# Optimization experiments

Measured on AMD Instinct MI355X. Metric: run time of the kernel, lower is better.

The kernel has to match this reference:

```python
import jax, jax.numpy as jnp
import numpy as np

N = 50000          # nodes
E_RAND = 590000    # random edges (+ N self-loops -> E = 640000)
IN_F = 128
OUT_F = 128
H, D = 8, 16       # num_heads, head_dim (H*D == OUT_F)
HOP = 5
ALPHA = 0.1
SLOPE = 0.2
EPS = 1e-5


def _layer_norm(x, g, b):
    mu = jnp.mean(x, axis=-1, keepdims=True)
    var = jnp.mean((x - mu) ** 2, axis=-1, keepdims=True)
    return (x - mu) * jax.lax.rsqrt(var + EPS) * g + b


def setup_inputs() -> dict:
    key = jax.random.key(0)
    ks = jax.random.split(key, 10)
    loops = jnp.arange(N, dtype=jnp.int32)  # self-loops -> no 0-in-degree nodes
    src = jnp.concatenate([loops, jax.random.randint(ks[0], (E_RAND,), 0, N, dtype=jnp.int32)])
    dst = jnp.concatenate([loops, jax.random.randint(ks[1], (E_RAND,), 0, N, dtype=jnp.int32)])
    s = 0.05  # xavier-like small init gain
    return {
        "feat": jax.random.normal(ks[2], (N, IN_F), jnp.float32),
        "src": src,
        "dst": dst,
        "w_head": jax.random.normal(ks[3], (OUT_F, IN_F), jnp.float32) * s,
        "w_tail": jax.random.normal(ks[4], (OUT_F, IN_F), jnp.float32) * s,
        "w_ent": jax.random.normal(ks[5], (OUT_F, IN_F), jnp.float32) * s,
        "attn": jax.random.normal(ks[6], (1, H, D), jnp.float32) * s,
        "ln1_g": jnp.ones((IN_F,), jnp.float32),
        "ln1_b": jnp.zeros((IN_F,), jnp.float32),
        "ln2_g": jnp.ones((OUT_F,), jnp.float32),
        "ln2_b": jnp.zeros((OUT_F,), jnp.float32),
        "ff_w1": jax.random.normal(ks[7], (4 * OUT_F, OUT_F), jnp.float32) * s,
        "ff_b1": jnp.zeros((4 * OUT_F,), jnp.float32),
        "ff_w2": jax.random.normal(ks[8], (OUT_F, 4 * OUT_F), jnp.float32) * s,
        "ff_b2": jnp.zeros((OUT_F,), jnp.float32),
    }


def _forward(src, dst, feat, w_head, w_tail, w_ent, attn,
             ln1_g, ln1_b, ln2_g, ln2_b, ff_w1, ff_b1, ff_w2, ff_b2):
    ones = jnp.ones(src.shape[0], jnp.float32)
    out_deg = jnp.clip(jax.ops.segment_sum(ones, src, num_segments=N), 1.0)  # [N]
    in_deg = jnp.clip(jax.ops.segment_sum(ones, dst, num_segments=N), 1.0)
    head_norm = out_deg ** -0.5
    tail_norm = in_deg ** 0.5
    log_in = jnp.log1p(in_deg)  # graph.dstdata['log_in'] (log of in-degree, set at graph build time)

    x = _layer_norm(feat, ln1_g, ln1_b)  # graph_layer_norm (feat_drop=0 in eval)
    fh = (x @ w_head.T).reshape(N, H, D) * head_norm[:, None, None]
    ft = (x @ w_tail.T).reshape(N, H, D) * head_norm[:, None, None]
    fe = (x @ w_ent.T).reshape(N, H, D) * head_norm[:, None, None]

    # edge attention logits: u_mul_v -> leaky_relu -> dot with attn vector
    lr = jax.nn.leaky_relu(fh[src] * ft[dst], SLOPE)  # [E,H,D]
    e = jnp.einsum('ehd,xhd->eh', lr, attn)           # [E,H]
    e = e * log_in[dst][:, None] / D                  # e_mul_v with log_in, / head_dim

    # edge softmax grouped by destination node, per head
    seg_max = jax.ops.segment_max(e, dst, num_segments=N)
    e_exp = jnp.exp(e - seg_max[dst])
    denom = jax.ops.segment_sum(e_exp, dst, num_segments=N)
    a = e_exp / denom[dst]                            # [E,H]

    # PPR diffusion (ppr_estimation), attn_drop=0 in eval
    feat0 = fe
    h = feat0
    for hop in range(HOP):
        if hop > 0:
            h = h * head_norm[:, None, None]
        m = h[src] * a[:, :, None]                    # [E,H,D] u_mul_e
        h = jax.ops.segment_sum(m, dst, num_segments=N)  # fn.sum
        h = h * tail_norm[:, None, None]
        h = (1.0 - ALPHA) * h + ALPHA * feat0

    rst = h + feat.reshape(N, H, D)  # res_fc is Identity since in_feats == out_feats
    rst = rst.reshape(N, OUT_F)
    ff = _layer_norm(rst, ln2_g, ln2_b)
    ff = jax.nn.relu(ff @ ff_w1.T + ff_b1) @ ff_w2.T + ff_b2  # PositionWiseFeedForward
    return ff + rst


def reference(feat, src, dst, w_head, w_tail, w_ent, attn, ln1_g, ln1_b,
              ln2_g, ln2_b, ff_w1, ff_b1, ff_w2, ff_b2):
    return _forward(src, dst, feat, w_head, w_tail, w_ent, attn,
                    ln1_g, ln1_b, ln2_g, ln2_b, ff_w1, ff_b1, ff_w2, ff_b2)
```

## Files before the change

### kernel.cpp

```cpp
#include <hip/hip_runtime.h>
#include <hip/hip_bf16.h>

typedef __attribute__((ext_vector_type(8))) short bf16x8;
typedef __attribute__((ext_vector_type(4))) float f32x4;
typedef unsigned int uint32;

#define F 128
#define HOPS 5
#define LDS_STRIDE 68
#define W1_STRIDE 136
#define W2_STRIDE 72
#define TB_STRIDE 72

__device__ __forceinline__ float b2f(__hip_bfloat16 h) { return __bfloat162float(h); }
__device__ __forceinline__ __hip_bfloat16 f2b(float f) { return __float2bfloat16(f); }

__device__ __forceinline__ float load_in(const void* p, size_t i, int isbf) {
    return isbf ? __bfloat162float(((const __hip_bfloat16*)p)[i]) : ((const float*)p)[i];
}

__device__ __forceinline__ float bflo(uint32 u) { union { uint32 i; float f; } v; v.i = u << 16; return v.f; }
__device__ __forceinline__ float bfhi(uint32 u) { union { uint32 i; float f; } v; v.i = u & 0xffff0000u; return v.f; }
__device__ __forceinline__ uint32 packbf2(float a, float b) {
    __hip_bfloat16 ha = f2b(a), hb = f2b(b);
    unsigned short ua = *(unsigned short*)&ha, ub = *(unsigned short*)&hb;
    return ((uint32)ub << 16) | ua;
}

__device__ __forceinline__ float edge_dot(uint4 gv, const float* ftf, const float* at) {
    float acc = 0.f;
    uint32 us[4] = {gv.x, gv.y, gv.z, gv.w};
    #pragma unroll
    for (int k = 0; k < 4; ++k) {
        float f0 = bflo(us[k]) * ftf[2 * k];
        float f1 = bfhi(us[k]) * ftf[2 * k + 1];
        f0 = fmaxf(f0, 0.2f * f0);
        f1 = fmaxf(f1, 0.2f * f1);
        acc = fmaf(f0, at[2 * k], acc);
        acc = fmaf(f1, at[2 * k + 1], acc);
    }
    return acc;
}

__global__ void detect_k(const uint32* __restrict__ w, int* flag) {
    __shared__ int cnt[256];
    int t = threadIdx.x;
    uint32 x = w[t * 97];
    int e_low = (x >> 7) & 0xFF;
    cnt[t] = (e_low >= 110 && e_low <= 135) ? 1 : 0;
    __syncthreads();
    for (int s = 128; s > 0; s >>= 1) {
        if (t < s) cnt[t] += cnt[t + s];
        __syncthreads();
    }
    if (t == 0) flag[0] = (cnt[0] >= 160) ? 1 : 0;
}

__global__ void cvt_all_k(const void* __restrict__ w_head, const void* __restrict__ w_tail,
                          const void* __restrict__ w_ent, const void* __restrict__ ff_w1,
                          const void* __restrict__ ff_w2, const void* __restrict__ attn,
                          const void* __restrict__ ff_b1, const void* __restrict__ ff_b2,
                          const int* __restrict__ flag,
                          __hip_bfloat16* __restrict__ wblob, float* __restrict__ fblob) {
    int i = blockIdx.x * blockDim.x + threadIdx.x;
    int isbf = flag[0];
    if (i < 180224) {
        const void* srcp; int j;
        if (i < 16384)       { srcp = w_head; j = i; }
        else if (i < 32768)  { srcp = w_tail; j = i - 16384; }
        else if (i < 49152)  { srcp = w_ent;  j = i - 32768; }
        else if (i < 114688) { srcp = ff_w1;  j = i - 49152; }
        else                 { srcp = ff_w2;  j = i - 114688; }
        wblob[i] = f2b(load_in(srcp, j, isbf));
    } else if (i < 180992) {
        int k = i - 180224;
        const void* srcp; int j;
        if (k < 128)      { srcp = attn;  j = k; }
        else if (k < 640) { srcp = ff_b1; j = k - 128; }
        else              { srcp = ff_b2; j = k - 640; }
        fblob[k] = load_in(srcp, j, isbf);
    }
}

__global__ void degree_k(const int* __restrict__ src, const int* __restrict__ dst,
                         int* in_cnt, int* out_cnt, int E) {
    int i = blockIdx.x * blockDim.x + threadIdx.x;
    if (i < E) {
        atomicAdd(&in_cnt[dst[i]], 1);
        atomicAdd(&out_cnt[src[i]], 1);
    }
}

__global__ void scan1_k(const int* __restrict__ cnt, int* partial, int* blk_sum, int N) {
    __shared__ int sh[256];
    int t = threadIdx.x;
    int i = blockIdx.x * 256 + t;
    int c = (i < N) ? cnt[i] : 0;
    sh[t] = c;
    __syncthreads();
    for (int o = 1; o < 256; o <<= 1) {
        int v = (t >= o) ? sh[t - o] : 0;
        __syncthreads();
        sh[t] += v;
        __syncthreads();
    }
    if (i < N) partial[i] = sh[t] - c;
    if (t == 255) blk_sum[blockIdx.x] = sh[255];
}

__global__ void scan2_k(const int* __restrict__ blk_sum, int* blk_off, int nb,
                        int* row_ptr, int N) {
    __shared__ int sh[256];
    int t = threadIdx.x;
    if (nb <= 256) {
        int v = (t < nb) ? blk_sum[t] : 0;
        sh[t] = v;
        __syncthreads();
        for (int o = 1; o < 256; o <<= 1) {
            int u = (t >= o) ? sh[t - o] : 0;
            __syncthreads();
            sh[t] += u;
            __syncthreads();
        }
        if (t < nb) blk_off[t] = sh[t] - v;
        if (t == 255) row_ptr[N] = sh[255];
    } else if (t == 0) {
        int run = 0;
        for (int b = 0; b < nb; ++b) { blk_off[b] = run; run += blk_sum[b]; }
        row_ptr[N] = run;
    }
}

__global__ void scan3_norms_k(const int* __restrict__ partial, const int* __restrict__ blk_off,
                              const int* __restrict__ cnt_in, const int* __restrict__ cnt_out,
                              int* row_ptr, float* head_norm, float* tail_norm,
                              float* log_in, int N) {
    int i = blockIdx.x * 256 + threadIdx.x;
    if (i >= N) return;
    row_ptr[i] = partial[i] + blk_off[blockIdx.x];
    float id = fmaxf((float)cnt_in[i], 1.0f);
    float od = fmaxf((float)cnt_out[i], 1.0f);
    head_norm[i] = rsqrtf(od);
    tail_norm[i] = sqrtf(id);
    log_in[i] = log1pf(id);
}

__global__ void scatter_k(const int* __restrict__ src, const int* __restrict__ dst,
                          const int* __restrict__ row_ptr, int* cursor,
                          int* csr_src, int E) {
    int i = blockIdx.x * blockDim.x + threadIdx.x;
    if (i < E) {
        int d = dst[i];
        int p = row_ptr[d] + atomicAdd(&cursor[d], 1);
        csr_src[p] = src[i];
    }
}

__global__ void ln1_k(const void* __restrict__ x, const void* __restrict__ g,
                      const void* __restrict__ b, const int* __restrict__ flag,
                      __hip_bfloat16* __restrict__ y, int N) {
    int w = blockIdx.x * (blockDim.x >> 6) + (threadIdx.x >> 6);
    if (w >= N) return;
    int isbf = flag[0];
    int t = threadIdx.x & 63;
    float v0 = load_in(x, (size_t)w * F + t, isbf);
    float v1 = load_in(x, (size_t)w * F + t + 64, isbf);
    float s = v0 + v1, sq = v0 * v0 + v1 * v1;
    for (int m = 1; m < 64; m <<= 1) { s += __shfl_xor(s, m, 64); sq += __shfl_xor(sq, m, 64); }
    float mu = s * (1.0f / F);
    float var = fmaxf(sq * (1.0f / F) - mu * mu, 0.0f);
    float r = rsqrtf(var + 1e-5f);
    y[(size_t)w * F + t]      = f2b((v0 - mu) * r * load_in(g, t, isbf) + load_in(b, t, isbf));
    y[(size_t)w * F + t + 64] = f2b((v1 - mu) * r * load_in(g, t + 64, isbf) + load_in(b, t + 64, isbf));
}

__global__ void ln2_k(const float* __restrict__ x, const void* __restrict__ g,
                      const void* __restrict__ b, const int* __restrict__ flag,
                      __hip_bfloat16* __restrict__ y, int N) {
    int w = blockIdx.x * (blockDim.x >> 6) + (threadIdx.x >> 6);
    if (w >= N) return;
    int isbf = flag[0];
    int t = threadIdx.x & 63;
    float v0 = x[(size_t)w * F + t], v1 = x[(size_t)w * F + t + 64];
    float s = v0 + v1, sq = v0 * v0 + v1 * v1;
    for (int m = 1; m < 64; m <<= 1) { s += __shfl_xor(s, m, 64); sq += __shfl_xor(sq, m, 64); }
    float mu = s * (1.0f / F);
    float var = fmaxf(sq * (1.0f / F) - mu * mu, 0.0f);
    float r = rsqrtf(var + 1e-5f);
    y[(size_t)w * F + t]      = f2b((v0 - mu) * r * load_in(g, t, isbf) + load_in(b, t, isbf));
    y[(size_t)w * F + t + 64] = f2b((v1 - mu) * r * load_in(g, t + 64, isbf) + load_in(b, t + 64, isbf));
}

__global__ void proj_gemm_k(const __hip_bfloat16* __restrict__ X,
                            const __hip_bfloat16* __restrict__ Wall,
                            const float* __restrict__ head_norm,
                            __hip_bfloat16* __restrict__ fh,
                            __hip_bfloat16* __restrict__ ft,
                            uint32* __restrict__ fe_bf, int N) {
    __shared__ __align__(16) char smem[2 * 64 * W1_STRIDE * 2];
    __hip_bfloat16* lx = (__hip_bfloat16*)smem;
    __hip_bfloat16* lw = (__hip_bfloat16*)(smem + 64 * W1_STRIDE * 2);
    float* eps = (float*)smem;
    int tid = threadIdx.x;
    int wv = tid >> 6, lane = tid & 63;
    int lr = lane & 15, quad = lane >> 4;
    int bm = blockIdx.x * 64;
    int g = blockIdx.y;
    int wsel = g >> 1;
    int wcb = (g & 1) * 64;
    {
        const __hip_bfloat16* xs = X + (size_t)bm * F;
        size_t maxe = (size_t)N * F;
#pragma unroll
        for (int i = 0; i < 4; ++i) {
            int idx = i * 2048 + tid * 8;
            int n = idx >> 7, k = idx & 127;
            size_t gi = (size_t)bm * F + idx;
            uint4 v = (gi + 8 <= maxe) ? *(const uint4*)(xs + idx)
                                       : *(const uint4*)(X + maxe - 8);
            *(uint4*)&lx[n * W1_STRIDE + k] = v;
        }
        const __hip_bfloat16* ws = Wall + ((size_t)wsel * F + wcb) * F;
#pragma unroll
        for (int i = 0; i < 4; ++i) {
            int idx = i * 2048 + tid * 8;
            int n = idx >> 7, k = idx & 127;
            *(uint4*)&lw[n * W1_STRIDE + k] = *(const uint4*)(ws + idx);
        }
    }
    __syncthreads();
    f32x4 acc[4] = {{0,0,0,0},{0,0,0,0},{0,0,0,0},{0,0,0,0}};
#pragma unroll
    for (int ks = 0; ks < 4; ++ks) {
        bf16x8 a = *reinterpret_cast<const bf16x8*>(&lx[(wv * 16 + lr) * W1_STRIDE + ks * 32 + quad * 8]);
#pragma unroll
        for (int j = 0; j < 4; ++j) {
            bf16x8 bb = *reinterpret_cast<const bf16x8*>(&lw[(j * 16 + lr) * W1_STRIDE + ks * 32 + quad * 8]);
            acc[j] = __builtin_amdgcn_mfma_f32_16x16x32_bf16(a, bb, acc[j], 0, 0, 0);
        }
    }
    __syncthreads();
    int rl = wv * 16 + quad * 4;
#pragma unroll
    for (int j = 0; j < 4; ++j)
#pragma unroll
        for (int r = 0; r < 4; ++r)
            eps[(rl + r) * LDS_STRIDE + j * 16 + lr] = acc[j][r];
    __syncthreads();
    int tr = tid >> 4, tc = (tid & 15) * 4;
#pragma unroll
    for (int p = 0; p < 4; ++p) {
        int row_l = p * 16 + tr;
        int grow = bm + row_l;
        if (grow >= N) continue;
        float4 v = *(const float4*)&eps[row_l * LDS_STRIDE + tc];
        float hn = head_norm[grow];
        v.x *= hn; v.y *= hn; v.z *= hn; v.w *= hn;
        size_t idx = (size_t)grow * F + wcb + tc;
        uint2 u; u.x = packbf2(v.x, v.y); u.y = packbf2(v.z, v.w);
        __hip_bfloat16* dstp = (wsel == 0) ? fh : (wsel == 1) ? ft : (__hip_bfloat16*)fe_bf;
        *(uint2*)&dstp[idx] = u;
    }
}

__global__ void attn_soft_k(const int* __restrict__ csr_src, const int* __restrict__ row_ptr,
                            const uint32* __restrict__ fh2, const uint32* __restrict__ ft2,
                            const float* __restrict__ attn_f, const float* __restrict__ log_in,
                            float* __restrict__ e_buf, float* __restrict__ inv_arr, int N) {
    int w = blockIdx.x * (blockDim.x >> 6) + (threadIdx.x >> 6);
    if (w >= N) return;
    int t = threadIdx.x & 63;
    int g = t >> 4, j = t & 15;
    int b = row_ptr[w], e = row_ptr[w + 1];
    uint4 fr = ((const uint4*)ft2)[(size_t)w * 16 + j];
    float ftf[8] = {bflo(fr.x), bfhi(fr.x), bflo(fr.y), bfhi(fr.y),
                    bflo(fr.z), bfhi(fr.z), bflo(fr.w), bfhi(fr.w)};
    float at[8];
#pragma unroll
    for (int k = 0; k < 8; ++k) at[k] = attn_f[8 * j + k];
    float scale = log_in[w] * (1.0f / 16.0f);
    float m = -1e30f;
    for (int p0 = b; p0 < e; p0 += 8) {
        int pa = p0 + g, pb = p0 + 4 + g;
        bool oka = pa < e, okb = pb < e;
        int sa = csr_src[oka ? pa : b];
        int sb = csr_src[okb ? pb : b];
        uint4 ga = ((const uint4*)fh2)[(size_t)sa * 16 + j];
        uint4 gb = ((const uint4*)fh2)[(size_t)sb * 16 + j];
        float ra = edge_dot(ga, ftf, at);
        float rb = edge_dot(gb, ftf, at);
        ra += __shfl_xor(ra, 1, 64);
        rb += __shfl_xor(rb, 1, 64);
        float la = ra * scale, lb = rb * scale;
        if (oka) { if (!(j & 1)) e_buf[(size_t)pa * 8 + (j >> 1)] = la; m = fmaxf(m, la); }
        if (okb) { if (!(j & 1)) e_buf[(size_t)pb * 8 + (j >> 1)] = lb; m = fmaxf(m, lb); }
    }
    m = fmaxf(m, __shfl_xor(m, 16, 64));
    m = fmaxf(m, __shfl_xor(m, 32, 64));
    float mh = __shfl(m, (t & 7) * 2, 64);
    float sum = 0.f;
    for (size_t base = (size_t)b * 8 + t; base < (size_t)e * 8; base += 64) {
        float ex = expf(e_buf[base] - mh);
        e_buf[base] = ex;
        sum += ex;
    }
    sum += __shfl_xor(sum, 8, 64);
    sum += __shfl_xor(sum, 16, 64);
    sum += __shfl_xor(sum, 32, 64);
    float inv = 1.0f / fmaxf(sum, 1e-30f);
    if (t < 8) inv_arr[(size_t)w * 8 + t] = inv;
}

__global__ void hop_k(const uint32* __restrict__ gsrc2, const float* __restrict__ e_exp,
                      const float* __restrict__ inv_arr,
                      const int* __restrict__ csr_src, const int* __restrict__ row_ptr,
                      const float* __restrict__ tail_norm, const float* __restrict__ head_norm,
                      const uint32* __restrict__ fe_bf, const void* __restrict__ feat,
                      const int* __restrict__ flag,
                      uint32* __restrict__ out_bf, float* __restrict__ out_f32,
                      int last, int N) {
    int w = blockIdx.x * (blockDim.x >> 6) + (threadIdx.x >> 6);
    if (w >= N) return;
    int t = threadIdx.x & 63;
    int sl = t >> 5, l = t & 31;
    int h = l >> 2;
    int b = row_ptr[w], e = row_ptr[w + 1];
    float inv = inv_arr[(size_t)w * 8 + h];
    float a0 = 0.f, a1 = 0.f, a2 = 0.f, a3 = 0.f;
    int p = b;
    for (; p + 8 <= e; p += 8) {
        int pe[4]; int s[4]; float av[4]; uint2 gg[4];
#pragma unroll
        for (int i = 0; i < 4; ++i) pe[i] = p + 2 * i + sl;
#pragma unroll
        for (int i = 0; i < 4; ++i) s[i] = csr_src[pe[i]];
#pragma unroll
        for (int i = 0; i < 4; ++i) av[i] = e_exp[(size_t)pe[i] * 8 + h];
#pragma unroll
        for (int i = 0; i < 4; ++i) gg[i] = ((const uint2*)gsrc2)[(size_t)s[i] * 32 + l];
#pragma unroll
        for (int i = 0; i < 4; ++i) {
            a0 += bflo(gg[i].x) * av[i]; a1 += bfhi(gg[i].x) * av[i];
            a2 += bflo(gg[i].y) * av[i]; a3 += bfhi(gg[i].y) * av[i];
        }
    }
    if (p < e) {
        int pe[4]; int s[4]; float av[4]; uint2 gg[4]; bool ok[4];
#pragma unroll
        for (int i = 0; i < 4; ++i) {
            int q = p + 2 * i + sl;
            ok[i] = q < e;
            pe[i] = ok[i] ? q : b;
        }
#pragma unroll
        for (int i = 0; i < 4; ++i) s[i] = csr_src[pe[i]];
#pragma unroll
        for (int i = 0; i < 4; ++i) av[i] = ok[i] ? e_exp[(size_t)pe[i] * 8 + h] : 0.f;
#pragma unroll
        for (int i = 0; i < 4; ++i) gg[i] = ((const uint2*)gsrc2)[(size_t)s[i] * 32 + l];
#pragma unroll
        for (int i = 0; i < 4; ++i) {
            a0 += bflo(gg[i].x) * av[i]; a1 += bfhi(gg[i].x) * av[i];
            a2 += bflo(gg[i].y) * av[i]; a3 += bfhi(gg[i].y) * av[i];
        }
    }
    a0 += __shfl_xor(a0, 32, 64);
    a1 += __shfl_xor(a1, 32, 64);
    a2 += __shfl_xor(a2, 32, 64);
    a3 += __shfl_xor(a3, 32, 64);
    if (t < 32) {
        float tl = tail_norm[w] * 0.9f * inv;
        uint2 feu = ((const uint2*)fe_bf)[(size_t)w * 32 + l];
        float r0 = tl * a0 + 0.1f * bflo(feu.x);
        float r1 = tl * a1 + 0.1f * bfhi(feu.x);
        float r2 = tl * a2 + 0.1f * bflo(feu.y);
        float r3 = tl * a3 + 0.1f * bfhi(feu.y);
        if (last) {
            int isbf = flag[0];
            float4 o;
            if (isbf) {
                uint2 fu = ((const uint2*)feat)[(size_t)w * 32 + l];
                o.x = r0 + bflo(fu.x); o.y = r1 + bfhi(fu.x);
                o.z = r2 + bflo(fu.y); o.w = r3 + bfhi(fu.y);
            } else {
                float4 fv = ((const float4*)feat)[(size_t)w * 32 + l];
                o.x = r0 + fv.x; o.y = r1 + fv.y; o.z = r2 + fv.z; o.w = r3 + fv.w;
            }
            ((float4*)out_f32)[(size_t)w * 32 + l] = o;
        } else {
            float hn = head_norm[w];
            uint2 u;
            u.x = packbf2(r0 * hn, r1 * hn);
            u.y = packbf2(r2 * hn, r3 * hn);
            ((uint2*)out_bf)[(size_t)w * 32 + l] = u;
        }
    }
}

__global__ __launch_bounds__(256, 2)
void ffn_fused_k(const __hip_bfloat16* __restrict__ Y, const __hip_bfloat16* __restrict__ W1,
                 const __hip_bfloat16* __restrict__ W2, const float* __restrict__ b1f,
                 const float* __restrict__ b2f, const float* __restrict__ rst,
                 const int* __restrict__ flag, void* __restrict__ out, int N) {
    __shared__ __align__(16) char smem[45056];
    __hip_bfloat16* lw1 = (__hip_bfloat16*)smem;
    __hip_bfloat16* lw2 = (__hip_bfloat16*)(smem + 17408);
    __hip_bfloat16* tb  = (__hip_bfloat16*)(smem + 35840);
    float* eps = (float*)smem;
    int tid = threadIdx.x;
    int wv = tid >> 6, lane = tid & 63;
    int lr = lane & 15, quad = lane >> 4;
    int bm = blockIdx.x * 64;
    int row_a = bm + wv * 16 + lr;
    if (row_a >= N) row_a = N - 1;
    bf16x8 ay[4];
    {
        const __hip_bfloat16* yr = Y + (size_t)row_a * F + quad * 8;
#pragma unroll
        for (int ks = 0; ks < 4; ++ks) ay[ks] = *reinterpret_cast<const bf16x8*>(yr + ks * 32);
    }
    f32x4 o[8];
#pragma unroll
    for (int j = 0; j < 8; ++j) o[j] = (f32x4){0,0,0,0};
    __hip_bfloat16* tbuf = tb + wv * (16 * TB_STRIDE);
    for (int c = 0; c < 8; ++c) {
        int nb0 = c * 64;
        __syncthreads();
        {
            const __hip_bfloat16* s1 = W1 + (size_t)nb0 * F;
#pragma unroll
            for (int i = 0; i < 4; ++i) {
                int idx = i * 2048 + tid * 8;
                int n = idx >> 7, k = idx & 127;
                *(uint4*)&lw1[n * W1_STRIDE + k] = *(const uint4*)(s1 + idx);
            }
#pragma unroll
            for (int i = 0; i < 4; ++i) {
                int idx = i * 2048 + tid * 8;
                int r = idx >> 6, k2 = idx & 63;
                *(uint4*)&lw2[r * W2_STRIDE + k2] = *(const uint4*)(W2 + (size_t)r * 512 + nb0 + k2);
            }
        }
        __syncthreads();
        f32x4 t[4] = {{0,0,0,0},{0,0,0,0},{0,0,0,0},{0,0,0,0}};
#pragma unroll
        for (int ks = 0; ks < 4; ++ks) {
#pragma unroll
            for (int j = 0; j < 4; ++j) {
                bf16x8 bb = *reinterpret_cast<const bf16x8*>(&lw1[(j * 16 + lr) * W1_STRIDE + ks * 32 + quad * 8]);
                t[j] = __builtin_amdgcn_mfma_f32_16x16x32_bf16(ay[ks], bb, t[j], 0, 0, 0);
            }
        }
#pragma unroll
        for (int j = 0; j < 4; ++j) {
            float bias = b1f[nb0 + 16 * j + lr];
#pragma unroll
            for (int r = 0; r < 4; ++r) {
                float v = fmaxf(t[j][r] + bias, 0.f);
                tbuf[(quad * 4 + r) * TB_STRIDE + j * 16 + lr] = f2b(v);
            }
        }
#pragma unroll
        for (int ks2 = 0; ks2 < 2; ++ks2) {
            bf16x8 at = *reinterpret_cast<const bf16x8*>(&tbuf[lr * TB_STRIDE + ks2 * 32 + quad * 8]);
#pragma unroll
            for (int j2 = 0; j2 < 8; ++j2) {
                bf16x8 bb = *reinterpret_cast<const bf16x8*>(&lw2[(j2 * 16 + lr) * W2_STRIDE + ks2 * 32 + quad * 8]);
                o[j2] = __builtin_amdgcn_mfma_f32_16x16x32_bf16(at, bb, o[j2], 0, 0, 0);
            }
        }
    }
    __syncthreads();
    int rl = wv * 16 + quad * 4;
#pragma unroll
    for (int j = 0; j < 8; ++j)
#pragma unroll
        for (int r = 0; r < 4; ++r)
            eps[(rl + r) * 132 + j * 16 + lr] = o[j][r];
    __syncthreads();
    int isbf = flag[0];
#pragma unroll
    for (int p = 0; p < 8; ++p) {
        int idx = p * 1024 + tid * 4;
        int row_l = idx >> 7, col = idx & 127;
        int grow = bm + row_l;
        if (grow >= N) continue;
        float4 v = *(const float4*)&eps[row_l * 132 + col];
        float4 bias = *(const float4*)&b2f[col];
        float4 rv = *(const float4*)&rst[(size_t)grow * F + col];
        v.x += bias.x + rv.x; v.y += bias.y + rv.y;
        v.z += bias.z + rv.z; v.w += bias.w + rv.w;
        size_t gidx = (size_t)grow * F + col;
        if (isbf) {
            uint2 u; u.x = packbf2(v.x, v.y); u.y = packbf2(v.z, v.w);
            *(uint2*)&((__hip_bfloat16*)out)[gidx] = u;
        } else {
            *(float4*)&((float*)out)[gidx] = v;
        }
    }
}

extern "C" void kernel_launch(void* const* d_in, const int* in_sizes, int n_in,
                              void* d_out, int out_size, void* d_ws, size_t ws_size,
                              hipStream_t stream) {
    if (n_in < 15) return;
    const void* feat = d_in[0];
    const int* src = (const int*)d_in[1];
    const int* dst = (const int*)d_in[2];
    const void* w_head = d_in[3];
    const void* w_tail = d_in[4];
    const void* w_ent  = d_in[5];
    const void* attn   = d_in[6];
    const void* ln1_g  = d_in[7];
    const void* ln1_b  = d_in[8];
    const void* ln2_g  = d_in[9];
    const void* ln2_b  = d_in[10];
    const void* ff_w1  = d_in[11];
    const void* ff_b1  = d_in[12];
    const void* ff_w2  = d_in[13];
    const void* ff_b2  = d_in[14];

    const int N = in_sizes[0] / F;
    const int E = in_sizes[1];
    (void)out_size;

    char* base = (char*)d_ws;
    size_t off = 0;
    auto alloc = [&](size_t bytes) -> void* {
        void* r = base + off;
        off += (bytes + 255) & ~(size_t)255;
        return r;
    };
    int* cnt3      = (int*)alloc((size_t)3 * N * 4);
    int* in_cnt = cnt3, * out_cnt = cnt3 + N, * cursor = cnt3 + 2 * N;
    int* row_ptr   = (int*)alloc((size_t)(N + 1) * 4);
    int* partial   = (int*)alloc((size_t)N * 4);
    int* blk_sum   = (int*)alloc((size_t)1024 * 4);
    int* blk_off   = (int*)alloc((size_t)1024 * 4);
    int* flag      = (int*)alloc(256);
    float* head_norm = (float*)alloc((size_t)N * 4);
    float* tail_norm = (float*)alloc((size_t)N * 4);
    float* log_in    = (float*)alloc((size_t)N * 4);
    float* inv_arr   = (float*)alloc((size_t)N * 8 * 4);
    int* csr_src   = (int*)alloc((size_t)E * 4);
    __hip_bfloat16* wh_bf = (__hip_bfloat16*)alloc((size_t)F * F * 2);
    __hip_bfloat16* wt_bf = (__hip_bfloat16*)alloc((size_t)F * F * 2);
    __hip_bfloat16* we_bf = (__hip_bfloat16*)alloc((size_t)F * F * 2);
    __hip_bfloat16* w1_bf = (__hip_bfloat16*)alloc((size_t)512 * F * 2);
    __hip_bfloat16* w2_bf = (__hip_bfloat16*)alloc((size_t)F * 512 * 2);
    float* attn_f    = (float*)alloc((size_t)F * 4);
    float* b1f       = (float*)alloc((size_t)512 * 4);
    float* b2f_      = (float*)alloc((size_t)F * 4);
    __hip_bfloat16* x_bf = (__hip_bfloat16*)alloc((size_t)N * F * 2);
    __hip_bfloat16* fh   = (__hip_bfloat16*)alloc((size_t)N * F * 2);
    __hip_bfloat16* ftb  = (__hip_bfloat16*)alloc((size_t)N * F * 2);
    float* e_a = (float*)alloc((size_t)E * 8 * 4);
    uint32* fe_bf = (uint32*)alloc((size_t)N * F * 2);
    uint32* hA_bf = (uint32*)alloc((size_t)N * F * 2);
    uint32* hB_bf = (uint32*)alloc((size_t)N * F * 2);
    float* rst = (float*)alloc((size_t)N * F * 4);
    __hip_bfloat16* y_bf = (__hip_bfloat16*)hA_bf;
    (void)wt_bf; (void)we_bf;
    if (off > ws_size) return;

    const int Mb = (N + 63) / 64;
    const int nodeBlocks = (N + 3) / 4;
    const int nb = (N + 255) / 256;

    detect_k<<<1, 256, 0, stream>>>((const uint32*)feat, flag);
    cvt_all_k<<<(180992 + 255) / 256, 256, 0, stream>>>(w_head, w_tail, w_ent, ff_w1, ff_w2,
                                                        attn, ff_b1, ff_b2, flag, wh_bf, attn_f);

    hipMemsetAsync(cnt3, 0, (size_t)3 * N * 4, stream);
    degree_k<<<(E + 255) / 256, 256, 0, stream>>>(src, dst, in_cnt, out_cnt, E);
    scan1_k<<<nb, 256, 0, stream>>>(in_cnt, partial, blk_sum, N);
    scan2_k<<<1, 256, 0, stream>>>(blk_sum, blk_off, nb, row_ptr, N);
    scan3_norms_k<<<nb, 256, 0, stream>>>(partial, blk_off, in_cnt, out_cnt,
                                          row_ptr, head_norm, tail_norm, log_in, N);
    scatter_k<<<(E + 255) / 256, 256, 0, stream>>>(src, dst, row_ptr, cursor, csr_src, E);

    ln1_k<<<nodeBlocks, 256, 0, stream>>>(feat, ln1_g, ln1_b, flag, x_bf, N);
    proj_gemm_k<<<dim3(Mb, 6), 256, 0, stream>>>(x_bf, wh_bf, head_norm, fh, ftb, fe_bf, N);

    attn_soft_k<<<nodeBlocks, 256, 0, stream>>>(csr_src, row_ptr, (const uint32*)fh,
                                                (const uint32*)ftb, attn_f, log_in,
                                                e_a, inv_arr, N);

    const uint32* gsrc = fe_bf;
    uint32* bufs[2] = {hA_bf, hB_bf};
    for (int hop = 0; hop < HOPS; ++hop) {
        int last = (hop == HOPS - 1);
        uint32* dst_bf = last ? nullptr : bufs[hop & 1];
        hop_k<<<nodeBlocks, 256, 0, stream>>>(gsrc, e_a, inv_arr, csr_src, row_ptr, tail_norm,
                                              head_norm, fe_bf, feat, flag, dst_bf, rst, last, N);
        if (!last) gsrc = dst_bf;
    }

    ln2_k<<<nodeBlocks, 256, 0, stream>>>(rst, ln2_g, ln2_b, flag, y_bf, N);
    ffn_fused_k<<<Mb, 256, 0, stream>>>(y_bf, w1_bf, w2_bf, b1f, b2f_, rst, flag, d_out, N);
}
```

Baseline: 472.4 us.

## Slice degree/scatter atomics into 8 partitions and use half-wave per node in hop

Degree counting and CSR scatter now spread their atomics over 8 per-block-slice counter arrays, so fewer threads contend on the same address. Per-slice offsets are computed in the scan kernel. The hop kernel now gives each node 32 lanes instead of 64, with each lane walking all 8 edges of a chunk, which removes the cross-half shuffle reduction and doubles the nodes per block. The cost is a larger memset plus extra scan reads, and a wider per-lane unroll that raises register pressure.

```diff
diff --git a/kernel.cpp b/kernel.cpp
--- a/kernel.cpp
+++ b/kernel.cpp
@@ -83,19 +83,24 @@
 }
 
 __global__ void degree_k(const int* __restrict__ src, const int* __restrict__ dst,
-                         int* in_cnt, int* out_cnt, int E) {
+                         int* in8, int* out8, int E, int N) {
     int i = blockIdx.x * blockDim.x + threadIdx.x;
+    int slice = blockIdx.x & 7;
     if (i < E) {
-        atomicAdd(&in_cnt[dst[i]], 1);
-        atomicAdd(&out_cnt[src[i]], 1);
-    }
-}
-
-__global__ void scan1_k(const int* __restrict__ cnt, int* partial, int* blk_sum, int N) {
+        atomicAdd(&in8[slice * N + dst[i]], 1);
+        atomicAdd(&out8[slice * N + src[i]], 1);
+    }
+}
+
+__global__ void scan1_k(const int* __restrict__ in8, int* partial, int* blk_sum, int N) {
     __shared__ int sh[256];
     int t = threadIdx.x;
     int i = blockIdx.x * 256 + t;
-    int c = (i < N) ? cnt[i] : 0;
+    int c = 0;
+    if (i < N) {
+#pragma unroll
+        for (int s = 0; s < 8; ++s) c += in8[s * N + i];
+    }
     sh[t] = c;
     __syncthreads();
     for (int o = 1; o < 256; o <<= 1) {
@@ -132,26 +137,33 @@
 }
 
 __global__ void scan3_norms_k(const int* __restrict__ partial, const int* __restrict__ blk_off,
-                              const int* __restrict__ cnt_in, const int* __restrict__ cnt_out,
-                              int* row_ptr, float* head_norm, float* tail_norm,
+                              const int* __restrict__ in8, const int* __restrict__ out8,
+                              int* row_ptr, int* soff, float* head_norm, float* tail_norm,
                               float* log_in, int N) {
     int i = blockIdx.x * 256 + threadIdx.x;
     if (i >= N) return;
     row_ptr[i] = partial[i] + blk_off[blockIdx.x];
-    float id = fmaxf((float)cnt_in[i], 1.0f);
-    float od = fmaxf((float)cnt_out[i], 1.0f);
-    head_norm[i] = rsqrtf(od);
+    int run = 0;
+#pragma unroll
+    for (int s = 0; s < 8; ++s) { soff[s * N + i] = run; run += in8[s * N + i]; }
+    int od = 0;
+#pragma unroll
+    for (int s = 0; s < 8; ++s) od += out8[s * N + i];
+    float id = fmaxf((float)run, 1.0f);
+    float odf = fmaxf((float)od, 1.0f);
+    head_norm[i] = rsqrtf(odf);
     tail_norm[i] = sqrtf(id);
     log_in[i] = log1pf(id);
 }
 
 __global__ void scatter_k(const int* __restrict__ src, const int* __restrict__ dst,
-                          const int* __restrict__ row_ptr, int* cursor,
-                          int* csr_src, int E) {
+                          const int* __restrict__ row_ptr, const int* __restrict__ soff,
+                          int* cursor8, int* csr_src, int E, int N) {
     int i = blockIdx.x * blockDim.x + threadIdx.x;
+    int slice = blockIdx.x & 7;
     if (i < E) {
         int d = dst[i];
-        int p = row_ptr[d] + atomicAdd(&cursor[d], 1);
+        int p = row_ptr[d] + soff[slice * N + d] + atomicAdd(&cursor8[slice * N + d], 1);
         csr_src[p] = src[i];
     }
 }
@@ -319,81 +331,70 @@
                       const int* __restrict__ flag,
                       uint32* __restrict__ out_bf, float* __restrict__ out_f32,
                       int last, int N) {
-    int w = blockIdx.x * (blockDim.x >> 6) + (threadIdx.x >> 6);
+    int w = blockIdx.x * 8 + (threadIdx.x >> 5);
     if (w >= N) return;
-    int t = threadIdx.x & 63;
-    int sl = t >> 5, l = t & 31;
+    int l = threadIdx.x & 31;
     int h = l >> 2;
     int b = row_ptr[w], e = row_ptr[w + 1];
     float inv = inv_arr[(size_t)w * 8 + h];
     float a0 = 0.f, a1 = 0.f, a2 = 0.f, a3 = 0.f;
     int p = b;
     for (; p + 8 <= e; p += 8) {
-        int pe[4]; int s[4]; float av[4]; uint2 gg[4];
-#pragma unroll
-        for (int i = 0; i < 4; ++i) pe[i] = p + 2 * i + sl;
-#pragma unroll
-        for (int i = 0; i < 4; ++i) s[i] = csr_src[pe[i]];
-#pragma unroll
-        for (int i = 0; i < 4; ++i) av[i] = e_exp[(size_t)pe[i] * 8 + h];
-#pragma unroll
-        for (int i = 0; i < 4; ++i) gg[i] = ((const uint2*)gsrc2)[(size_t)s[i] * 32 + l];
-#pragma unroll
-        for (int i = 0; i < 4; ++i) {
+        int s[8]; float av[8]; uint2 gg[8];
+#pragma unroll
+        for (int i = 0; i < 8; ++i) s[i] = csr_src[p + i];
+#pragma unroll
+        for (int i = 0; i < 8; ++i) av[i] = e_exp[(size_t)(p + i) * 8 + h];
+#pragma unroll
+        for (int i = 0; i < 8; ++i) gg[i] = ((const uint2*)gsrc2)[(size_t)s[i] * 32 + l];
+#pragma unroll
+        for (int i = 0; i < 8; ++i) {
             a0 += bflo(gg[i].x) * av[i]; a1 += bfhi(gg[i].x) * av[i];
             a2 += bflo(gg[i].y) * av[i]; a3 += bfhi(gg[i].y) * av[i];
         }
     }
     if (p < e) {
-        int pe[4]; int s[4]; float av[4]; uint2 gg[4]; bool ok[4];
-#pragma unroll
-        for (int i = 0; i < 4; ++i) {
-            int q = p + 2 * i + sl;
-            ok[i] = q < e;
-            pe[i] = ok[i] ? q : b;
-        }
-#pragma unroll
-        for (int i = 0; i < 4; ++i) s[i] = csr_src[pe[i]];
-#pragma unroll
-        for (int i = 0; i < 4; ++i) av[i] = ok[i] ? e_exp[(size_t)pe[i] * 8 + h] : 0.f;
-#pragma unroll
-        for (int i = 0; i < 4; ++i) gg[i] = ((const uint2*)gsrc2)[(size_t)s[i] * 32 + l];
-#pragma unroll
-        for (int i = 0; i < 4; ++i) {
+        int s[8]; float av[8]; uint2 gg[8];
+#pragma unroll
+        for (int i = 0; i < 8; ++i) {
+            int q = p + i;
+            bool ok = q < e;
+            int q2 = ok ? q : b;
+            s[i] = csr_src[q2];
+            av[i] = ok ? e_exp[(size_t)q * 8 + h] : 0.f;
+        }
+#pragma unroll
+        for (int i = 0; i < 8; ++i) gg[i] = ((const uint2*)gsrc2)[(size_t)s[i] * 32 + l];
+#pragma unroll
+        for (int i = 0; i < 8; ++i) {
             a0 += bflo(gg[i].x) * av[i]; a1 += bfhi(gg[i].x) * av[i];
             a2 += bflo(gg[i].y) * av[i]; a3 += bfhi(gg[i].y) * av[i];
         }
     }
-    a0 += __shfl_xor(a0, 32, 64);
-    a1 += __shfl_xor(a1, 32, 64);
-    a2 += __shfl_xor(a2, 32, 64);
-    a3 += __shfl_xor(a3, 32, 64);
-    if (t < 32) {
-        float tl = tail_norm[w] * 0.9f * inv;
-        uint2 feu = ((const uint2*)fe_bf)[(size_t)w * 32 + l];
-        float r0 = tl * a0 + 0.1f * bflo(feu.x);
-        float r1 = tl * a1 + 0.1f * bfhi(feu.x);
-        float r2 = tl * a2 + 0.1f * bflo(feu.y);
-        float r3 = tl * a3 + 0.1f * bfhi(feu.y);
-        if (last) {
-            int isbf = flag[0];
-            float4 o;
-            if (isbf) {
-                uint2 fu = ((const uint2*)feat)[(size_t)w * 32 + l];
-                o.x = r0 + bflo(fu.x); o.y = r1 + bfhi(fu.x);
-                o.z = r2 + bflo(fu.y); o.w = r3 + bfhi(fu.y);
-            } else {
-                float4 fv = ((const float4*)feat)[(size_t)w * 32 + l];
-                o.x = r0 + fv.x; o.y = r1 + fv.y; o.z = r2 + fv.z; o.w = r3 + fv.w;
-            }
-            ((float4*)out_f32)[(size_t)w * 32 + l] = o;
+    float tl = tail_norm[w] * 0.9f * inv;
+    uint2 feu = ((const uint2*)fe_bf)[(size_t)w * 32 + l];
+    float r0 = tl * a0 + 0.1f * bflo(feu.x);
+    float r1 = tl * a1 + 0.1f * bfhi(feu.x);
+    float r2 = tl * a2 + 0.1f * bflo(feu.y);
+    float r3 = tl * a3 + 0.1f * bfhi(feu.y);
+    if (last) {
+        int isbf = flag[0];
+        float4 o;
+        if (isbf) {
+            uint2 fu = ((const uint2*)feat)[(size_t)w * 32 + l];
+            o.x = r0 + bflo(fu.x); o.y = r1 + bfhi(fu.x);
+            o.z = r2 + bflo(fu.y); o.w = r3 + bfhi(fu.y);
         } else {
-            float hn = head_norm[w];
-            uint2 u;
-            u.x = packbf2(r0 * hn, r1 * hn);
-            u.y = packbf2(r2 * hn, r3 * hn);
-            ((uint2*)out_bf)[(size_t)w * 32 + l] = u;
-        }
+            float4 fv = ((const float4*)feat)[(size_t)w * 32 + l];
+            o.x = r0 + fv.x; o.y = r1 + fv.y; o.z = r2 + fv.z; o.w = r3 + fv.w;
+        }
+        ((float4*)out_f32)[(size_t)w * 32 + l] = o;
+    } else {
+        float hn = head_norm[w];
+        uint2 u;
+        u.x = packbf2(r0 * hn, r1 * hn);
+        u.y = packbf2(r2 * hn, r3 * hn);
+        ((uint2*)out_bf)[(size_t)w * 32 + l] = u;
     }
 }
 
@@ -531,8 +532,9 @@
         off += (bytes + 255) & ~(size_t)255;
         return r;
     };
-    int* cnt3      = (int*)alloc((size_t)3 * N * 4);
-    int* in_cnt = cnt3, * out_cnt = cnt3 + N, * cursor = cnt3 + 2 * N;
+    int* zr        = (int*)alloc((size_t)24 * N * 4);
+    int* in8 = zr, * out8 = zr + 8 * N, * cursor8 = zr + 16 * N;
+    int* soff      = (int*)alloc((size_t)8 * N * 4);
     int* row_ptr   = (int*)alloc((size_t)(N + 1) * 4);
     int* partial   = (int*)alloc((size_t)N * 4);
     int* blk_sum   = (int*)alloc((size_t)1024 * 4);
@@ -565,19 +567,20 @@
 
     const int Mb = (N + 63) / 64;
     const int nodeBlocks = (N + 3) / 4;
+    const int hopBlocks = (N + 7) / 8;
     const int nb = (N + 255) / 256;
 
     detect_k<<<1, 256, 0, stream>>>((const uint32*)feat, flag);
     cvt_all_k<<<(180992 + 255) / 256, 256, 0, stream>>>(w_head, w_tail, w_ent, ff_w1, ff_w2,
                                                         attn, ff_b1, ff_b2, flag, wh_bf, attn_f);
 
-    hipMemsetAsync(cnt3, 0, (size_t)3 * N * 4, stream);
-    degree_k<<<(E + 255) / 256, 256, 0, stream>>>(src, dst, in_cnt, out_cnt, E);
-    scan1_k<<<nb, 256, 0, stream>>>(in_cnt, partial, blk_sum, N);
+    hipMemsetAsync(zr, 0, (size_t)24 * N * 4, stream);
+    degree_k<<<(E + 255) / 256, 256, 0, stream>>>(src, dst, in8, out8, E, N);
+    scan1_k<<<nb, 256, 0, stream>>>(in8, partial, blk_sum, N);
     scan2_k<<<1, 256, 0, stream>>>(blk_sum, blk_off, nb, row_ptr, N);
-    scan3_norms_k<<<nb, 256, 0, stream>>>(partial, blk_off, in_cnt, out_cnt,
-                                          row_ptr, head_norm, tail_norm, log_in, N);
-    scatter_k<<<(E + 255) / 256, 256, 0, stream>>>(src, dst, row_ptr, cursor, csr_src, E);
+    scan3_norms_k<<<nb, 256, 0, stream>>>(partial, blk_off, in8, out8,
+                                          row_ptr, soff, head_norm, tail_norm, log_in, N);
+    scatter_k<<<(E + 255) / 256, 256, 0, stream>>>(src, dst, row_ptr, soff, cursor8, csr_src, E, N);
 
     ln1_k<<<nodeBlocks, 256, 0, stream>>>(feat, ln1_g, ln1_b, flag, x_bf, N);
     proj_gemm_k<<<dim3(Mb, 6), 256, 0, stream>>>(x_bf, wh_bf, head_norm, fh, ftb, fe_bf, N);
@@ -591,8 +594,8 @@
     for (int hop = 0; hop < HOPS; ++hop) {
         int last = (hop == HOPS - 1);
         uint32* dst_bf = last ? nullptr : bufs[hop & 1];
-        hop_k<<<nodeBlocks, 256, 0, stream>>>(gsrc, e_a, inv_arr, csr_src, row_ptr, tail_norm,
-                                              head_norm, fe_bf, feat, flag, dst_bf, rst, last, N);
+        hop_k<<<hopBlocks, 256, 0, stream>>>(gsrc, e_a, inv_arr, csr_src, row_ptr, tail_norm,
+                                             head_norm, fe_bf, feat, flag, dst_bf, rst, last, N);
         if (!last) gsrc = dst_bf;
     }
 
```

Result: no change. 467.8 us (-1.0%).
